# Performance work log

Hardware: AMD Instinct MI355X
Metric: run time of the kernel (lower is better)

The kernel has to match this reference:

```python
import jax, jax.numpy as jnp
import numpy as np
from jax import lax

T, B, S, D = 16, 8, 256, 1024
M, H = 1024, 8
HD = M // H
TAU_MEM = 0.99
TAU_GATE = 0.9
VTH = 1.0
LN_EPS = 1e-5


def lif(inp, tau, vth):
    """LIF over leading time axis. inp: (T, N, M). Returns (spikes, membrane trace)."""
    def step(v, i):
        v = tau * v + i                      # integrate with leak
        s = (v >= vth).astype(i.dtype)       # hard threshold spike
        return v - s * vth, (s, v)           # subtract reset; trace is pre-reset membrane
    v0 = jnp.zeros(inp.shape[1:], inp.dtype)
    _, (spikes, mv) = lax.scan(step, v0, inp)
    return spikes, mv


def setup_inputs() -> dict:
    key = jax.random.key(0)
    ks = jax.random.split(key, 6)
    inp = {
        "x": jax.random.normal(ks[0], (T, B, S, D), dtype=jnp.float32),
        "W_to_memory": jax.random.normal(ks[1], (M, D), dtype=jnp.float32) / np.sqrt(D),
        "W_gate": jax.random.normal(ks[2], (M, D), dtype=jnp.float32) / np.sqrt(D),
        "W_read_key": jax.random.normal(ks[3], (M, M), dtype=jnp.float32) / np.sqrt(M),
        "W_from_memory": jax.random.normal(ks[4], (D, M), dtype=jnp.float32) / np.sqrt(M),
        "read_query": jax.random.normal(ks[5], (H, HD), dtype=jnp.float32) * 0.02,
        "gate_threshold": jnp.float32(0.5),
        "ln_gamma": jnp.ones((D,), jnp.float32),
        "ln_beta": jnp.zeros((D,), jnp.float32),
        "memory_mix": jnp.float32(0.1),
    }
    return inp


def reference(x, W_to_memory, W_gate, W_read_key, W_from_memory, read_query,
              gate_threshold, ln_gamma, ln_beta, memory_mix):
    N = B * S
    xf = x.reshape(T, N, D)

    # memory write path
    mi = jnp.einsum('tnd,md->tnm', xf, W_to_memory)        # (T,N,M)
    ms, mv = lif(mi, TAU_MEM, VTH)

    # spike-gated write
    gi = jnp.einsum('tnd,md->tnm', xf, W_gate)
    gs, _ = lif(gi, TAU_GATE, VTH)
    gate_sig = gs.mean(axis=0)                              # (N,M)
    gate_mask = jax.nn.sigmoid((gate_sig - gate_threshold) * 10.0)

    # multi-head temporal attention over T
    mvh = mv.reshape(T, N, H, HD)
    mk = jnp.einsum('tnm,km->tnk', mv, W_read_key).reshape(T, N, H, HD)
    scale = 1.0 / np.sqrt(HD)
    attn_s = jnp.einsum('tnhd,hd->tnh', mk, read_query) * scale
    attn_w = jax.nn.softmax(attn_s.astype(jnp.float32), axis=0).astype(mv.dtype)
    mem_read = jnp.einsum('tnhd,tnh->nhd', mvh, attn_w).reshape(N, M)
    mem_read = mem_read * gate_mask

    # project back, layernorm, residual mix
    mem_out = jnp.einsum('nm,dm->nd', mem_read, W_from_memory).astype(jnp.float32)
    mu = mem_out.mean(axis=-1, keepdims=True)
    var = mem_out.var(axis=-1, keepdims=True)
    mem_out = (mem_out - mu) * lax.rsqrt(var + LN_EPS) * ln_gamma + ln_beta
    mem_out = mem_out.astype(x.dtype)

    mix = jax.nn.sigmoid(memory_mix)
    x_enhanced = x + mix * mem_out.reshape(1, B, S, D)
    return x_enhanced
```

## Files before the change

### kernel.cpp

```cpp
#include <hip/hip_runtime.h>
#include <hip/hip_bf16.h>
#include <hip/hip_fp16.h>

#define TT 16
#define NN 2048
#define DD 1024
#define MM 1024
#define HH 8
#define ROWS 32768
#define JJ 2048

typedef _Float16 f16x8 __attribute__((ext_vector_type(8)));
typedef float f32x4 __attribute__((ext_vector_type(4)));

#define SB  __builtin_amdgcn_sched_barrier(0)
#define BAR __builtin_amdgcn_s_barrier()

__device__ __forceinline__ void gload16(const void* g, void* l) {
    __builtin_amdgcn_global_load_lds((const __attribute__((address_space(1))) void*)g,
                                     (__attribute__((address_space(3))) void*)l, 16, 0, 0);
}

__global__ __launch_bounds__(256) void pack_hi(const float* __restrict__ in,
                                               __half* __restrict__ hi, long n4) {
    long i = (long)blockIdx.x * 256 + threadIdx.x;
    if (i >= n4) return;
    float4 v = ((const float4*)in)[i];
    ushort4 H = { __half_as_ushort(__float2half(v.x)), __half_as_ushort(__float2half(v.y)),
                  __half_as_ushort(__float2half(v.z)), __half_as_ushort(__float2half(v.w)) };
    ((ushort4*)hi)[i] = H;
}

__global__ __launch_bounds__(256) void pack_hilo(const float* __restrict__ in,
                                                 __half* __restrict__ hi,
                                                 __half* __restrict__ lo, long n4) {
    long i = (long)blockIdx.x * 256 + threadIdx.x;
    if (i >= n4) return;
    float4 v = ((const float4*)in)[i];
    __half h0 = __float2half(v.x), h1 = __float2half(v.y);
    __half h2 = __float2half(v.z), h3 = __float2half(v.w);
    __half l0 = __float2half(v.x - __half2float(h0));
    __half l1 = __float2half(v.y - __half2float(h1));
    __half l2 = __float2half(v.z - __half2float(h2));
    __half l3 = __float2half(v.w - __half2float(h3));
    ushort4 H = { __half_as_ushort(h0), __half_as_ushort(h1), __half_as_ushort(h2), __half_as_ushort(h3) };
    ushort4 L = { __half_as_ushort(l0), __half_as_ushort(l1), __half_as_ushort(l2), __half_as_ushort(l3) };
    ((ushort4*)hi)[i] = H;
    ((ushort4*)lo)[i] = L;
}

__global__ __launch_bounds__(256) void compute_wq(const float* __restrict__ Wrk,
                                                  const float* __restrict__ q,
                                                  float* __restrict__ wq) {
    int m = blockIdx.x * 256 + threadIdx.x;
    int h = blockIdx.y;
    const float* qh = q + h * 128;
    const float* wr = Wrk + (size_t)h * 128 * MM + m;
    float acc = 0.f;
    for (int hd = 0; hd < 128; hd++) acc = fmaf(qh[hd], wr[(size_t)hd * MM], acc);
    wq[h * MM + m] = acc * 0.08838834764831845f;
}

__global__ __launch_bounds__(512, 2)
void gemm8p(const __half* __restrict__ Ahi, const __half* __restrict__ Alo,
            const __half* __restrict__ Bhi, const __half* __restrict__ Blo,
            float* __restrict__ C)
{
    extern __shared__ __align__(16) char smem[];
    char* AHb = smem;
    char* ALb = smem + 32768;
    char* BHb = smem + 65536;
    char* BLb = smem + 98304;

    const int tid = threadIdx.x, lane = tid & 63, wave = tid >> 6;
    const int l15 = lane & 15, l4 = lane >> 4;
    const int wm = wave >> 2, wn = wave & 3;

    const int orig = blockIdx.x;
    const int wg   = (orig & 7) * 128 + (orig >> 3);
    const int rb   = (wg >> 3) * 256;
    const int cb   = (wg & 7) * 256;

    auto stageU = [&](const __half* src, int row0, char* dstbase, int par, int kt, int s) {
        int t   = s * 512 + tid;
        int row = t >> 2;
        int p   = t & 3;
        int kb  = (p ^ ((row >> 1) & 3)) * 16;
        const char* g = (const char*)(src + (size_t)(row0 + row) * 1024 + kt * 32) + kb;
        gload16(g, dstbase + par * 16384 + (size_t)(s * 512 + wave * 64) * 16);
    };
    auto rdT = [&](const char* base, int par, int row) -> f16x8 {
        int p = l4 ^ ((row >> 1) & 3);
        return *(const f16x8*)(base + par * 16384 + row * 64 + p * 16);
    };

    f32x4 acc[8][4] = {};
    const int NKT = 32;

    stageU(Ahi, rb, AHb, 0, 0, 0); stageU(Ahi, rb, AHb, 0, 0, 1);
    stageU(Alo, rb, ALb, 0, 0, 0); stageU(Alo, rb, ALb, 0, 0, 1);
    stageU(Bhi, cb, BHb, 0, 0, 0); stageU(Bhi, cb, BHb, 0, 0, 1);
    stageU(Blo, cb, BLb, 0, 0, 0); stageU(Blo, cb, BLb, 0, 0, 1);
    asm volatile("s_waitcnt vmcnt(2)" ::: "memory");
    SB; BAR;

    for (int kt = 0; kt < NKT; kt++) {
        const int p = kt & 1, pn = p ^ 1;
        const bool pre = (kt + 1 < NKT);
        f16x8 a[8], bh[4], bl[4];

        #pragma unroll
        for (int i = 0; i < 8; i++) a[i] = rdT(AHb, p, wm * 128 + i * 16 + l15);
        #pragma unroll
        for (int n = 0; n < 4; n++) bh[n] = rdT(BHb, p, wn * 64 + n * 16 + l15);
        if (pre) { stageU(Ahi, rb, AHb, pn, kt + 1, 0); stageU(Ahi, rb, AHb, pn, kt + 1, 1); }
        SB; BAR;
        __builtin_amdgcn_s_setprio(1);
        #pragma unroll
        for (int i = 0; i < 4; i++)
            #pragma unroll
            for (int n = 0; n < 4; n++)
                acc[i][n] = __builtin_amdgcn_mfma_f32_16x16x32_f16(a[i], bh[n], acc[i][n], 0, 0, 0);
        __builtin_amdgcn_s_setprio(0);
        SB; BAR;

        if (pre) { stageU(Alo, rb, ALb, pn, kt + 1, 0); stageU(Alo, rb, ALb, pn, kt + 1, 1); }
        SB; BAR;
        __builtin_amdgcn_s_setprio(1);
        #pragma unroll
        for (int i = 0; i < 4; i++)
            #pragma unroll
            for (int n = 0; n < 4; n++)
                acc[4 + i][n] = __builtin_amdgcn_mfma_f32_16x16x32_f16(a[4 + i], bh[n], acc[4 + i][n], 0, 0, 0);
        __builtin_amdgcn_s_setprio(0);
        SB;
        if (pre) asm volatile("s_waitcnt vmcnt(4)" ::: "memory");
        else     asm volatile("s_waitcnt vmcnt(0)" ::: "memory");
        SB; BAR;

        #pragma unroll
        for (int n = 0; n < 4; n++) bl[n] = rdT(BLb, p, wn * 64 + n * 16 + l15);
        if (pre) { stageU(Bhi, cb, BHb, pn, kt + 1, 0); stageU(Bhi, cb, BHb, pn, kt + 1, 1); }
        SB; BAR;
        __builtin_amdgcn_s_setprio(1);
        #pragma unroll
        for (int i = 0; i < 4; i++)
            #pragma unroll
            for (int n = 0; n < 4; n++)
                acc[i][n] = __builtin_amdgcn_mfma_f32_16x16x32_f16(a[i], bl[n], acc[i][n], 0, 0, 0);
        __builtin_amdgcn_s_setprio(0);
        SB; BAR;

        if (pre) { stageU(Blo, cb, BLb, pn, kt + 1, 0); stageU(Blo, cb, BLb, pn, kt + 1, 1); }
        SB; BAR;
        __builtin_amdgcn_s_setprio(1);
        #pragma unroll
        for (int i = 0; i < 4; i++)
            #pragma unroll
            for (int n = 0; n < 4; n++)
                acc[4 + i][n] = __builtin_amdgcn_mfma_f32_16x16x32_f16(a[4 + i], bl[n], acc[4 + i][n], 0, 0, 0);
        __builtin_amdgcn_s_setprio(0);
        SB; BAR;

        #pragma unroll
        for (int i = 0; i < 8; i++) a[i] = rdT(ALb, p, wm * 128 + i * 16 + l15);
        SB; BAR;
        __builtin_amdgcn_s_setprio(1);
        #pragma unroll
        for (int i = 0; i < 4; i++)
            #pragma unroll
            for (int n = 0; n < 4; n++)
                acc[i][n] = __builtin_amdgcn_mfma_f32_16x16x32_f16(a[i], bh[n], acc[i][n], 0, 0, 0);
        __builtin_amdgcn_s_setprio(0);
        SB; BAR;

        __builtin_amdgcn_s_setprio(1);
        #pragma unroll
        for (int i = 0; i < 4; i++)
            #pragma unroll
            for (int n = 0; n < 4; n++)
                acc[4 + i][n] = __builtin_amdgcn_mfma_f32_16x16x32_f16(a[4 + i], bh[n], acc[4 + i][n], 0, 0, 0);
        __builtin_amdgcn_s_setprio(0);
        SB;
        asm volatile("s_waitcnt vmcnt(2)" ::: "memory");
        SB; BAR;
    }

    #pragma unroll
    for (int i = 0; i < 8; i++) {
        int r0 = rb + wm * 128 + i * 16 + l4 * 4;
        #pragma unroll
        for (int nf = 0; nf < 4; nf++) {
            int c = cb + wn * 64 + nf * 16 + l15;
            #pragma unroll
            for (int reg = 0; reg < 4; reg++)
                C[(size_t)(r0 + reg) * JJ + c] = acc[i][nf][reg];
        }
    }
}

template<int TERMS>
__global__ __launch_bounds__(256, 2)
void gemm_f16(const __half* __restrict__ Ahi, const __half* __restrict__ Alo,
              const __half* __restrict__ Bhi, const __half* __restrict__ Blo,
              float* __restrict__ C, int K, int ldc, int ncb_log2)
{
    __shared__ __align__(16) __half lds[2][4][8][512];
    const int tid  = threadIdx.x;
    const int lane = tid & 63;
    const int wave = tid >> 6;
    const int l15  = lane & 15, l4 = lane >> 4;

    const int nwg  = gridDim.x;
    const int orig = blockIdx.x;
    const int wg   = (orig & 7) * (nwg >> 3) + (orig >> 3);
    const int rb = (wg >> ncb_log2) * 128;
    const int cb = (wg & ((1 << ncb_log2) - 1)) * 128;

    auto stage = [&](int buf, int ks) {
        const int k0 = ks * 32;
        #pragma unroll
        for (int qq = 0; qq < 2; qq++) {
            int g = wave * 2 + qq;
            size_t aoff = (size_t)(rb + g * 16 + l15) * K + (k0 + 8 * l4);
            gload16(Ahi + aoff, &lds[buf][0][g][0]);
            if constexpr (TERMS == 3) gload16(Alo + aoff, &lds[buf][1][g][0]);
            size_t boff = (size_t)(cb + g * 16 + l15) * K + (k0 + 8 * l4);
            gload16(Bhi + boff, &lds[buf][2][g][0]);
            if constexpr (TERMS == 3) gload16(Blo + boff, &lds[buf][3][g][0]);
        }
    };

    const int wave_r = (wave >> 1) * 64;
    const int wave_c = (wave & 1) * 64;
    const int ag0 = wave_r >> 4;
    const int bg0 = wave_c >> 4;

    f32x4 acc[4][4] = {};
    const int nks = K >> 5;
    stage(0, 0);
    int buf = 0;
    for (int ks = 0; ks < nks; ks++) {
        __syncthreads();
        if (ks + 1 < nks) stage(buf ^ 1, ks + 1);
        f16x8 ah[4], bh[4], al[4], bl[4];
        #pragma unroll
        for (int i = 0; i < 4; i++) {
            ah[i] = *(const f16x8*)&lds[buf][0][ag0 + i][lane * 8];
            bh[i] = *(const f16x8*)&lds[buf][2][bg0 + i][lane * 8];
            if constexpr (TERMS == 3) {
                al[i] = *(const f16x8*)&lds[buf][1][ag0 + i][lane * 8];
                bl[i] = *(const f16x8*)&lds[buf][3][bg0 + i][lane * 8];
            }
        }
        #pragma unroll
        for (int m = 0; m < 4; m++)
            #pragma unroll
            for (int n = 0; n < 4; n++) {
                acc[m][n] = __builtin_amdgcn_mfma_f32_16x16x32_f16(ah[m], bh[n], acc[m][n], 0, 0, 0);
                if constexpr (TERMS == 3) {
                    acc[m][n] = __builtin_amdgcn_mfma_f32_16x16x32_f16(ah[m], bl[n], acc[m][n], 0, 0, 0);
                    acc[m][n] = __builtin_amdgcn_mfma_f32_16x16x32_f16(al[m], bh[n], acc[m][n], 0, 0, 0);
                }
            }
        buf ^= 1;
    }
    #pragma unroll
    for (int m = 0; m < 4; m++)
        #pragma unroll
        for (int n = 0; n < 4; n++) {
            int r0 = rb + wave_r + m * 16 + l4 * 4;
            int c  = cb + wave_c + n * 16 + l15;
            #pragma unroll
            for (int reg = 0; reg < 4; reg++)
                C[(size_t)(r0 + reg) * ldc + c] = acc[m][n][reg];
        }
}

__global__ __launch_bounds__(256)
void lif_kernel(const float* __restrict__ mi_gi, __half* __restrict__ mv,
                float* __restrict__ gmask, const float* __restrict__ gate_thr)
{
    int idx = blockIdx.x * 256 + threadIdx.x;
    int n = idx >> 10, m = idx & 1023;
    const float* pm = mi_gi + (size_t)n * JJ + m;
    const size_t tstride = (size_t)NN * JJ;
    __half* pv = mv + idx;
    float vm = 0.f, vg = 0.f, cnt = 0.f;
    #pragma unroll
    for (int t = 0; t < TT; t++) {
        float im = pm[(size_t)t * tstride];
        vm = 0.99f * vm + im;
        pv[(size_t)t * (NN * MM)] = __float2half(vm);
        if (vm >= 1.0f) vm -= 1.0f;
        float ig = pm[(size_t)t * tstride + MM];
        vg = 0.9f * vg + ig;
        if (vg >= 1.0f) { vg -= 1.0f; cnt += 1.0f; }
    }
    float gs = cnt * 0.0625f;
    gmask[idx] = 1.0f / (1.0f + expf(-10.0f * (gs - gate_thr[0])));
}

__global__ __launch_bounds__(256)
void attn_memread(const __half* __restrict__ mv, const float* __restrict__ wq,
                  const float* __restrict__ gmask, __half* __restrict__ mem_read)
{
    int n = blockIdx.x;
    __shared__ __align__(16) __half smv[TT][1032];
    __shared__ float sw[HH][TT];
    __shared__ float ssm[HH][TT];
    int tid = threadIdx.x;

    for (int t = 0; t < TT; t++) {
        const ushort4* src = (const ushort4*)(mv + ((size_t)t * NN + n) * MM);
        ((ushort4*)&smv[t][0])[tid] = src[tid];
    }
    __syncthreads();

    if (tid < 128) {
        int h = tid >> 4, t = tid & 15;
        const float* w = wq + h * MM;
        float acc = 0.f;
        for (int m = 0; m < MM; m += 2) {
            float2 v = __half22float2(*(const __half2*)&smv[t][m]);
            acc = fmaf(v.x, w[m], acc);
            acc = fmaf(v.y, w[m + 1], acc);
        }
        sw[h][t] = acc;
    }
    __syncthreads();
    if (tid < 8) {
        int h = tid;
        float mx = -1e30f;
        for (int t = 0; t < TT; t++) mx = fmaxf(mx, sw[h][t]);
        float s = 0.f;
        for (int t = 0; t < TT; t++) { float e = __expf(sw[h][t] - mx); ssm[h][t] = e; s += e; }
        float inv = 1.0f / s;
        for (int t = 0; t < TT; t++) ssm[h][t] *= inv;
    }
    __syncthreads();

    const float* gm = gmask + (size_t)n * MM;
    #pragma unroll
    for (int mm = 0; mm < 4; mm++) {
        int m = tid + mm * 256;
        int h = m >> 7;
        float acc = 0.f;
        #pragma unroll
        for (int t = 0; t < TT; t++) acc = fmaf(__half2float(smv[t][m]), ssm[h][t], acc);
        acc *= gm[m];
        mem_read[(size_t)n * MM + m] = __float2half(acc);
    }
}

__global__ __launch_bounds__(256)
void ln_add(const float* __restrict__ mem_out, const float* __restrict__ x,
            const float* __restrict__ gamma, const float* __restrict__ beta,
            const float* __restrict__ mmix, float* __restrict__ out)
{
    int n = blockIdx.x, tid = threadIdx.x;
    int lane = tid & 63, wave = tid >> 6;
    __shared__ float sred[10];
    float4 v = ((const float4*)(mem_out + (size_t)n * DD))[tid];
    float s  = v.x + v.y + v.z + v.w;
    float ss = v.x * v.x + v.y * v.y + v.z * v.z + v.w * v.w;
    #pragma unroll
    for (int o = 32; o > 0; o >>= 1) { s += __shfl_down(s, o, 64); ss += __shfl_down(ss, o, 64); }
    if (lane == 0) { sred[wave * 2] = s; sred[wave * 2 + 1] = ss; }
    __syncthreads();
    if (tid == 0) {
        float S = 0.f, SS = 0.f;
        for (int w = 0; w < 4; w++) { S += sred[w * 2]; SS += sred[w * 2 + 1]; }
        float mu = S * (1.0f / DD);
        float var = SS * (1.0f / DD) - mu * mu;
        sred[8] = mu;
        sred[9] = rsqrtf(var + 1e-5f);
    }
    __syncthreads();
    float mu = sred[8], rs = sred[9];
    float4 g = ((const float4*)gamma)[tid];
    float4 b = ((const float4*)beta)[tid];
    float4 nv;
    nv.x = (v.x - mu) * rs * g.x + b.x;
    nv.y = (v.y - mu) * rs * g.y + b.y;
    nv.z = (v.z - mu) * rs * g.z + b.z;
    nv.w = (v.w - mu) * rs * g.w + b.w;
    float mix = 1.0f / (1.0f + expf(-mmix[0]));
    for (int t = 0; t < TT; t++) {
        size_t off = ((size_t)t * NN + n) * DD;
        float4 xv = ((const float4*)(x + off))[tid];
        float4 o;
        o.x = xv.x + mix * nv.x;
        o.y = xv.y + mix * nv.y;
        o.z = xv.z + mix * nv.z;
        o.w = xv.w + mix * nv.w;
        ((float4*)(out + off))[tid] = o;
    }
}

__global__ void ws_sentinel(float* out) { out[0] = 12345.0f; }

extern "C" void kernel_launch(void* const* d_in, const int* in_sizes, int n_in,
                              void* d_out, int out_size, void* d_ws, size_t ws_size,
                              hipStream_t stream)
{
    const float* x     = (const float*)d_in[0];
    const float* Wto   = (const float*)d_in[1];
    const float* Wg    = (const float*)d_in[2];
    const float* Wrk   = (const float*)d_in[3];
    const float* Wfrom = (const float*)d_in[4];
    const float* q     = (const float*)d_in[5];
    const float* gthr  = (const float*)d_in[6];
    const float* gamma = (const float*)d_in[7];
    const float* beta  = (const float*)d_in[8];
    const float* mmix  = (const float*)d_in[9];
    float* out = (float*)d_out;

    char* w = (char*)d_ws;
    size_t off = 0;
    auto alloc = [&](size_t bytes) -> void* {
        void* p = w + off;
        off += (bytes + 255) & ~(size_t)255;
        return p;
    };
    __half* x_hi   = (__half*)alloc((size_t)ROWS * DD * 2);
    __half* x_lo   = (__half*)alloc((size_t)ROWS * DD * 2);
    __half* wc_hi  = (__half*)alloc((size_t)JJ * DD * 2);
    __half* wc_lo  = (__half*)alloc((size_t)JJ * DD * 2);
    __half* wf_hi  = (__half*)alloc((size_t)DD * MM * 2);
    float*  wq     = (float*) alloc((size_t)HH * MM * 4);
    float*  mi_gi  = (float*) alloc((size_t)ROWS * JJ * 4);
    __half* mv     = (__half*)alloc((size_t)TT * NN * MM * 2);
    float*  gmask  = (float*) alloc((size_t)NN * MM * 4);
    __half* m_read = (__half*)alloc((size_t)NN * MM * 2);
    float*  m_out  = (float*) alloc((size_t)NN * DD * 4);

    if (off > ws_size) {
        ws_sentinel<<<1, 1, 0, stream>>>(out);
        return;
    }

    hipFuncSetAttribute((const void*)gemm8p, hipFuncAttributeMaxDynamicSharedMemorySize, 131072);

    pack_hilo<<<(ROWS * DD / 4 + 255) / 256, 256, 0, stream>>>(x, x_hi, x_lo, ROWS * DD / 4);
    pack_hilo<<<(MM * DD / 4 + 255) / 256, 256, 0, stream>>>(Wto, wc_hi, wc_lo, MM * DD / 4);
    pack_hilo<<<(MM * DD / 4 + 255) / 256, 256, 0, stream>>>(Wg, wc_hi + (size_t)MM * DD, wc_lo + (size_t)MM * DD, MM * DD / 4);
    pack_hi<<<(DD * MM / 4 + 255) / 256, 256, 0, stream>>>(Wfrom, wf_hi, DD * MM / 4);
    compute_wq<<<dim3(4, 8), 256, 0, stream>>>(Wrk, q, wq);

    gemm8p<<<(ROWS / 256) * (JJ / 256), 512, 131072, stream>>>(x_hi, x_lo, wc_hi, wc_lo, mi_gi);

    lif_kernel<<<NN * MM / 256, 256, 0, stream>>>(mi_gi, mv, gmask, gthr);

    attn_memread<<<NN, 256, 0, stream>>>(mv, wq, gmask, m_read);

    gemm_f16<1><<<(NN / 128) * (DD / 128), 256, 0, stream>>>(m_read, m_read, wf_hi, wf_hi, m_out, MM, DD, 3);

    ln_add<<<NN, 256, 0, stream>>>(m_out, x, gamma, beta, mmix, out);
}
```

Measured before the change: 593.3 us.

## Collapse split-phase GEMM main loop to one barrier per K-iteration

Restructures the double-buffered f16 hi/lo split GEMM main loop. The fine-grained schedule had about ten block barriers, sched_barriers and partial vmcnt waits per iteration, with MFMA work split into half-tiles between them. It now does one vmcnt(0) plus one barrier at the top of each iteration, issues all next-tile prefetches in two groups, and runs full 8x4 MFMA batches. The aim is to cut barrier and synchronisation overhead and let the compiler schedule more freely. The trade-off is weaker explicit load/compute interleaving and a full memory wait each iteration, which could expose global-load latency.

```diff
diff --git a/kernel.cpp b/kernel.cpp
--- a/kernel.cpp
+++ b/kernel.cpp
@@ -101,89 +101,54 @@
     stageU(Alo, rb, ALb, 0, 0, 0); stageU(Alo, rb, ALb, 0, 0, 1);
     stageU(Bhi, cb, BHb, 0, 0, 0); stageU(Bhi, cb, BHb, 0, 0, 1);
     stageU(Blo, cb, BLb, 0, 0, 0); stageU(Blo, cb, BLb, 0, 0, 1);
-    asm volatile("s_waitcnt vmcnt(2)" ::: "memory");
-    SB; BAR;
 
     for (int kt = 0; kt < NKT; kt++) {
         const int p = kt & 1, pn = p ^ 1;
         const bool pre = (kt + 1 < NKT);
         f16x8 a[8], bh[4], bl[4];
 
+        asm volatile("s_waitcnt vmcnt(0)" ::: "memory");
+        SB; BAR;
+
         #pragma unroll
         for (int i = 0; i < 8; i++) a[i] = rdT(AHb, p, wm * 128 + i * 16 + l15);
         #pragma unroll
         for (int n = 0; n < 4; n++) bh[n] = rdT(BHb, p, wn * 64 + n * 16 + l15);
-        if (pre) { stageU(Ahi, rb, AHb, pn, kt + 1, 0); stageU(Ahi, rb, AHb, pn, kt + 1, 1); }
-        SB; BAR;
+        if (pre) {
+            stageU(Ahi, rb, AHb, pn, kt + 1, 0); stageU(Ahi, rb, AHb, pn, kt + 1, 1);
+            stageU(Alo, rb, ALb, pn, kt + 1, 0); stageU(Alo, rb, ALb, pn, kt + 1, 1);
+        }
         __builtin_amdgcn_s_setprio(1);
         #pragma unroll
-        for (int i = 0; i < 4; i++)
+        for (int i = 0; i < 8; i++)
             #pragma unroll
             for (int n = 0; n < 4; n++)
                 acc[i][n] = __builtin_amdgcn_mfma_f32_16x16x32_f16(a[i], bh[n], acc[i][n], 0, 0, 0);
         __builtin_amdgcn_s_setprio(0);
-        SB; BAR;
-
-        if (pre) { stageU(Alo, rb, ALb, pn, kt + 1, 0); stageU(Alo, rb, ALb, pn, kt + 1, 1); }
-        SB; BAR;
+
+        #pragma unroll
+        for (int n = 0; n < 4; n++) bl[n] = rdT(BLb, p, wn * 64 + n * 16 + l15);
+        if (pre) {
+            stageU(Bhi, cb, BHb, pn, kt + 1, 0); stageU(Bhi, cb, BHb, pn, kt + 1, 1);
+            stageU(Blo, cb, BLb, pn, kt + 1, 0); stageU(Blo, cb, BLb, pn, kt + 1, 1);
+        }
         __builtin_amdgcn_s_setprio(1);
         #pragma unroll
-        for (int i = 0; i < 4; i++)
-            #pragma unroll
-            for (int n = 0; n < 4; n++)
-                acc[4 + i][n] = __builtin_amdgcn_mfma_f32_16x16x32_f16(a[4 + i], bh[n], acc[4 + i][n], 0, 0, 0);
-        __builtin_amdgcn_s_setprio(0);
-        SB;
-        if (pre) asm volatile("s_waitcnt vmcnt(4)" ::: "memory");
-        else     asm volatile("s_waitcnt vmcnt(0)" ::: "memory");
-        SB; BAR;
-
-        #pragma unroll
-        for (int n = 0; n < 4; n++) bl[n] = rdT(BLb, p, wn * 64 + n * 16 + l15);
-        if (pre) { stageU(Bhi, cb, BHb, pn, kt + 1, 0); stageU(Bhi, cb, BHb, pn, kt + 1, 1); }
-        SB; BAR;
-        __builtin_amdgcn_s_setprio(1);
-        #pragma unroll
-        for (int i = 0; i < 4; i++)
+        for (int i = 0; i < 8; i++)
             #pragma unroll
             for (int n = 0; n < 4; n++)
                 acc[i][n] = __builtin_amdgcn_mfma_f32_16x16x32_f16(a[i], bl[n], acc[i][n], 0, 0, 0);
         __builtin_amdgcn_s_setprio(0);
-        SB; BAR;
-
-        if (pre) { stageU(Blo, cb, BLb, pn, kt + 1, 0); stageU(Blo, cb, BLb, pn, kt + 1, 1); }
-        SB; BAR;
+
+        #pragma unroll
+        for (int i = 0; i < 8; i++) a[i] = rdT(ALb, p, wm * 128 + i * 16 + l15);
         __builtin_amdgcn_s_setprio(1);
         #pragma unroll
-        for (int i = 0; i < 4; i++)
-            #pragma unroll
-            for (int n = 0; n < 4; n++)
-                acc[4 + i][n] = __builtin_amdgcn_mfma_f32_16x16x32_f16(a[4 + i], bl[n], acc[4 + i][n], 0, 0, 0);
-        __builtin_amdgcn_s_setprio(0);
-        SB; BAR;
-
-        #pragma unroll
-        for (int i = 0; i < 8; i++) a[i] = rdT(ALb, p, wm * 128 + i * 16 + l15);
-        SB; BAR;
-        __builtin_amdgcn_s_setprio(1);
-        #pragma unroll
-        for (int i = 0; i < 4; i++)
+        for (int i = 0; i < 8; i++)
             #pragma unroll
             for (int n = 0; n < 4; n++)
                 acc[i][n] = __builtin_amdgcn_mfma_f32_16x16x32_f16(a[i], bh[n], acc[i][n], 0, 0, 0);
         __builtin_amdgcn_s_setprio(0);
-        SB; BAR;
-
-        __builtin_amdgcn_s_setprio(1);
-        #pragma unroll
-        for (int i = 0; i < 4; i++)
-            #pragma unroll
-            for (int n = 0; n < 4; n++)
-                acc[4 + i][n] = __builtin_amdgcn_mfma_f32_16x16x32_f16(a[4 + i], bh[n], acc[4 + i][n], 0, 0, 0);
-        __builtin_amdgcn_s_setprio(0);
-        SB;
-        asm volatile("s_waitcnt vmcnt(2)" ::: "memory");
-        SB; BAR;
     }
 
     #pragma unroll
```

Result: no change. 583.8 us (-1.6%).
